# Kernel tuning notes

Measured on AMD Instinct MI355X. Metric: run time of the kernel, lower is better.

The kernel has to match this reference:

```python
import jax, jax.numpy as jnp
import numpy as np

B, T, DIN, DOUT, RANK, UDIM = 4, 2048, 4096, 4096, 2, 16

def setup_inputs() -> dict:
    key = jax.random.key(0)
    ks = jax.random.split(key, 8)
    return {
        "x": jax.random.normal(ks[0], (B, T, DIN), jnp.float32),
        "W": jax.random.normal(ks[1], (DOUT, DIN), jnp.float32) * 0.02,
        "b": jax.random.normal(ks[2], (DOUT,), jnp.float32) * 0.02,
        "U": jax.random.normal(ks[3], (DOUT, RANK), jnp.float32) * 0.02,
        "S": jax.random.normal(ks[4], (RANK, RANK), jnp.float32),
        "Vh": jax.random.normal(ks[5], (RANK, DIN), jnp.float32) * 0.02,
        "P": jax.random.normal(ks[6], (UDIM, RANK, RANK), jnp.float32),
        "v": jax.random.normal(ks[7], (UDIM,), jnp.float32),
    }

def reference(x, W, b, U, S, Vh, P, v):
    # R = sum_u v[u] * P[u]  (intended meaning of einsum('u,urr->rr'))
    R = jnp.einsum('u,uab->ab', v, P)                 # [rank, rank]
    base = jnp.einsum('btd,od->bto', x, W) + b        # frozen linear
    # x @ delta_W.T with delta_W = U @ S @ R @ Vh, chained low-rank:
    M = U @ S @ R                                     # [out, rank]
    t = jnp.einsum('btd,rd->btr', x, Vh)              # [B, T, rank]
    delta = jnp.einsum('btr,or->bto', t, M)           # [B, T, out]
    return base + delta
```

## Files before the change

kernel.cpp:

```cpp
#include <hip/hip_runtime.h>
#include <hip/hip_bf16.h>
#include <stdint.h>

typedef __hip_bfloat16 bf16;
typedef __attribute__((ext_vector_type(8))) short bf16x8;
typedef __attribute__((ext_vector_type(4))) float f32x4;

static constexpr int Mtot = 8192;
static constexpr int Ktot = 4096;
static constexpr int Ntot = 4096;
static constexpr int BM = 128, BN = 128, BK = 32;
static constexpr int NK = Ktot / BK;
static constexpr int CAST_BLOCKS = (Mtot * Ktot / 8) / 256;
static constexpr int PREP_BLOCKS = (Ntot * Ktot / 8) / 256;

__device__ __forceinline__ void gl_lds16(const void* g, void* l) {
  __builtin_amdgcn_global_load_lds(
      (const __attribute__((address_space(1))) void*)g,
      (__attribute__((address_space(3))) void*)l,
      16, 0, 0);
}

__device__ __forceinline__ uint32_t bf16pair(float a, float b) {
  __hip_bfloat16 ha = __float2bfloat16(a), hb = __float2bfloat16(b);
  uint16_t ia, ib;
  __builtin_memcpy(&ia, &ha, 2);
  __builtin_memcpy(&ib, &hb, 2);
  return (uint32_t)ia | ((uint32_t)ib << 16);
}

__global__ __launch_bounds__(256) void prep_kernel(const float* __restrict__ x,
                                                   bf16* __restrict__ xb,
                                                   const float* __restrict__ W,
                                                   const float* __restrict__ U,
                                                   const float* __restrict__ S,
                                                   const float* __restrict__ Vh,
                                                   const float* __restrict__ P,
                                                   const float* __restrict__ v,
                                                   bf16* __restrict__ Wp) {
  const int bid = blockIdx.x;
  if (bid < CAST_BLOCKS) {
    size_t gid = (size_t)bid * 256 + threadIdx.x;
    size_t d0 = gid * 8;
    const float4 a = ((const float4*)(x + d0))[0];
    const float4 b = ((const float4*)(x + d0))[1];
    uint4 pk;
    pk.x = bf16pair(a.x, a.y);
    pk.y = bf16pair(a.z, a.w);
    pk.z = bf16pair(b.x, b.y);
    pk.w = bf16pair(b.z, b.w);
    ((uint4*)(xb + d0))[0] = pk;
  } else {
    float R0 = 0.f, R1 = 0.f, R2 = 0.f, R3 = 0.f;
#pragma unroll
    for (int u = 0; u < 16; ++u) {
      float vu = v[u];
      R0 += vu * P[u * 4 + 0];
      R1 += vu * P[u * 4 + 1];
      R2 += vu * P[u * 4 + 2];
      R3 += vu * P[u * 4 + 3];
    }
    float SR00 = S[0] * R0 + S[1] * R2, SR01 = S[0] * R1 + S[1] * R3;
    float SR10 = S[2] * R0 + S[3] * R2, SR11 = S[2] * R1 + S[3] * R3;

    int gid = (bid - CAST_BLOCKS) * 256 + threadIdx.x;
    int o = gid >> 9;
    int d0 = (gid & 511) << 3;
    float u0 = U[o * 2 + 0], u1 = U[o * 2 + 1];
    float M0 = u0 * SR00 + u1 * SR10;
    float M1 = u0 * SR01 + u1 * SR11;

    const float* wrow = W + (size_t)o * Ktot + d0;
    const float4 w0 = ((const float4*)wrow)[0];
    const float4 w1 = ((const float4*)wrow)[1];
    const float4 a0 = ((const float4*)(Vh + d0))[0];
    const float4 a1 = ((const float4*)(Vh + d0))[1];
    const float4 b0 = ((const float4*)(Vh + Ktot + d0))[0];
    const float4 b1 = ((const float4*)(Vh + Ktot + d0))[1];
    float val[8];
    val[0] = w0.x + M0 * a0.x + M1 * b0.x;
    val[1] = w0.y + M0 * a0.y + M1 * b0.y;
    val[2] = w0.z + M0 * a0.z + M1 * b0.z;
    val[3] = w0.w + M0 * a0.w + M1 * b0.w;
    val[4] = w1.x + M0 * a1.x + M1 * b1.x;
    val[5] = w1.y + M0 * a1.y + M1 * b1.y;
    val[6] = w1.z + M0 * a1.z + M1 * b1.z;
    val[7] = w1.w + M0 * a1.w + M1 * b1.w;
    uint4 pk;
    pk.x = bf16pair(val[0], val[1]);
    pk.y = bf16pair(val[2], val[3]);
    pk.z = bf16pair(val[4], val[5]);
    pk.w = bf16pair(val[6], val[7]);
    ((uint4*)(Wp + (size_t)o * Ktot + d0))[0] = pk;
  }
}

__global__ __launch_bounds__(256) void gemm_kernel(const bf16* __restrict__ A,
                                                   const bf16* __restrict__ Bt,
                                                   const float* __restrict__ bias,
                                                   float* __restrict__ out) {
  __shared__ __align__(16) bf16 As[2][BM * BK];
  __shared__ __align__(16) bf16 Bs[2][BN * BK];

  const int tid = threadIdx.x;
  const int lane = tid & 63;
  const int wv = tid >> 6;
  const int m0 = blockIdx.y * BM;
  const int n0 = blockIdx.x * BN;

  const int lrow = lane >> 2;
  const int lk = (((lane & 3) ^ ((lrow >> 1) & 3)) << 3);

  const bf16* ga0 = A + (size_t)(m0 + wv * 32 + lrow) * Ktot + lk;
  const bf16* ga1 = ga0 + (size_t)16 * Ktot;
  const bf16* gb0 = Bt + (size_t)(n0 + wv * 32 + lrow) * Ktot + lk;
  const bf16* gb1 = gb0 + (size_t)16 * Ktot;
  const int laoff0 = (wv * 32) * BK;
  const int laoff1 = (wv * 32 + 16) * BK;

  const int moff = (wv >> 1) * 64;
  const int noff = (wv & 1) * 64;
  const int fm = lane & 15;
  const int q = lane >> 4;
  const int sw = ((q ^ ((fm >> 1) & 3)) << 3);

  f32x4 acc[4][4];
#pragma unroll
  for (int i = 0; i < 4; ++i)
#pragma unroll
    for (int j = 0; j < 4; ++j) acc[i][j] = {0.f, 0.f, 0.f, 0.f};

  gl_lds16(ga0, &As[0][laoff0]);
  gl_lds16(ga1, &As[0][laoff1]);
  gl_lds16(gb0, &Bs[0][laoff0]);
  gl_lds16(gb1, &Bs[0][laoff1]);
  ga0 += BK; ga1 += BK; gb0 += BK; gb1 += BK;
  __syncthreads();

  for (int kt = 0; kt < NK; ++kt) {
    const int cur = kt & 1;
    if (kt + 1 < NK) {
      const int nxt = cur ^ 1;
      gl_lds16(ga0, &As[nxt][laoff0]);
      gl_lds16(ga1, &As[nxt][laoff1]);
      gl_lds16(gb0, &Bs[nxt][laoff0]);
      gl_lds16(gb1, &Bs[nxt][laoff1]);
      ga0 += BK; ga1 += BK; gb0 += BK; gb1 += BK;
    }

    const bf16* pa = &As[cur][0];
    const bf16* pb = &Bs[cur][0];
    bf16x8 av[4], bv[4];
#pragma unroll
    for (int i = 0; i < 4; ++i)
      av[i] = *(const bf16x8*)(pa + (moff + i * 16 + fm) * BK + sw);
#pragma unroll
    for (int j = 0; j < 4; ++j)
      bv[j] = *(const bf16x8*)(pb + (noff + j * 16 + fm) * BK + sw);
#pragma unroll
    for (int i = 0; i < 4; ++i)
#pragma unroll
      for (int j = 0; j < 4; ++j)
        acc[i][j] = __builtin_amdgcn_mfma_f32_16x16x32_bf16(av[i], bv[j], acc[i][j], 0, 0, 0);

    __syncthreads();
  }

#pragma unroll
  for (int j = 0; j < 4; ++j) {
    const int gn = n0 + noff + j * 16 + fm;
    const float bj = bias[gn];
#pragma unroll
    for (int i = 0; i < 4; ++i) {
      const int gm = m0 + moff + i * 16 + q * 4;
#pragma unroll
      for (int r = 0; r < 4; ++r) {
        out[(size_t)(gm + r) * Ntot + gn] = acc[i][j][r] + bj;
      }
    }
  }
}

extern "C" void kernel_launch(void* const* d_in, const int* in_sizes, int n_in,
                              void* d_out, int out_size, void* d_ws, size_t ws_size,
                              hipStream_t stream) {
  const float* x  = (const float*)d_in[0];
  const float* W  = (const float*)d_in[1];
  const float* b  = (const float*)d_in[2];
  const float* U  = (const float*)d_in[3];
  const float* S  = (const float*)d_in[4];
  const float* Vh = (const float*)d_in[5];
  const float* P  = (const float*)d_in[6];
  const float* v  = (const float*)d_in[7];
  float* out = (float*)d_out;

  bf16* xb = (bf16*)d_ws;
  bf16* Wp = (bf16*)((char*)d_ws + (size_t)Mtot * Ktot * 2);

  prep_kernel<<<CAST_BLOCKS + PREP_BLOCKS, 256, 0, stream>>>(x, xb, W, U, S, Vh, P, v, Wp);

  dim3 grid(Ntot / BN, Mtot / BM);
  gemm_kernel<<<grid, 256, 0, stream>>>(xb, Wp, b, out);
}
```

Measured before the change: 621.6 us.

## Rewrite GEMM with 256x256x64 tiles, 8 waves, and finely interleaved ping-pong pipeline

The bf16 GEMM is restructured to use 256x256 tiles with BK=64 and 512 threads (8 waves, 2x4 layout, 128x64 per wave). Loads are staged as quarter-tiles interleaved with MFMA quadrants, synchronised by explicit barriers, waitcnts, sched_barriers and setprio. Blocks are remapped through an XCD-aware swizzle and a new XOR LDS swizzle is applied. This aims to raise arithmetic intensity and overlap global-to-LDS traffic with MFMA work, at the cost of higher register pressure, many barriers, and fragile hand-scheduled wait counts.

```diff
diff --git a/kernel.cpp b/kernel.cpp
--- a/kernel.cpp
+++ b/kernel.cpp
@@ -9,8 +9,8 @@
 static constexpr int Mtot = 8192;
 static constexpr int Ktot = 4096;
 static constexpr int Ntot = 4096;
-static constexpr int BM = 128, BN = 128, BK = 32;
-static constexpr int NK = Ktot / BK;
+static constexpr int BM = 256, BN = 256, BK = 64;
+static constexpr int NKT = Ktot / BK;
 static constexpr int CAST_BLOCKS = (Mtot * Ktot / 8) / 256;
 static constexpr int PREP_BLOCKS = (Ntot * Ktot / 8) / 256;
 
@@ -95,90 +95,154 @@
   }
 }
 
-__global__ __launch_bounds__(256) void gemm_kernel(const bf16* __restrict__ A,
-                                                   const bf16* __restrict__ Bt,
-                                                   const float* __restrict__ bias,
-                                                   float* __restrict__ out) {
+
+#define SCHEDB __builtin_amdgcn_sched_barrier(0)
+#define BAR do { SCHEDB; __builtin_amdgcn_s_barrier(); SCHEDB; } while (0)
+#define LG0 do { asm volatile("s_waitcnt lgkmcnt(0)" ::: "memory"); SCHEDB; } while (0)
+#define LG8 do { asm volatile("s_waitcnt lgkmcnt(8)" ::: "memory"); } while (0)
+#define WVM(n) do { asm volatile("s_waitcnt vmcnt(" #n ")" ::: "memory"); } while (0)
+
+__global__ __launch_bounds__(512, 2) void gemm_kernel(const bf16* __restrict__ A,
+                                                      const bf16* __restrict__ Bt,
+                                                      const float* __restrict__ bias,
+                                                      float* __restrict__ out) {
   __shared__ __align__(16) bf16 As[2][BM * BK];
   __shared__ __align__(16) bf16 Bs[2][BN * BK];
 
-  const int tid = threadIdx.x;
+  const int tid = (int)threadIdx.x;
   const int lane = tid & 63;
-  const int wv = tid >> 6;
-  const int m0 = blockIdx.y * BM;
-  const int n0 = blockIdx.x * BN;
-
-  const int lrow = lane >> 2;
-  const int lk = (((lane & 3) ^ ((lrow >> 1) & 3)) << 3);
-
-  const bf16* ga0 = A + (size_t)(m0 + wv * 32 + lrow) * Ktot + lk;
-  const bf16* ga1 = ga0 + (size_t)16 * Ktot;
-  const bf16* gb0 = Bt + (size_t)(n0 + wv * 32 + lrow) * Ktot + lk;
-  const bf16* gb1 = gb0 + (size_t)16 * Ktot;
-  const int laoff0 = (wv * 32) * BK;
-  const int laoff1 = (wv * 32 + 16) * BK;
-
-  const int moff = (wv >> 1) * 64;
-  const int noff = (wv & 1) * 64;
+  const int w = tid >> 6;
+  const int wr = w >> 2;
+  const int wc = w & 3;
+
+  int bid = (int)blockIdx.x;
+  bid = (bid & 7) * 64 + (bid >> 3);
+  const int m0 = (bid >> 4) * BM;
+  const int n0 = (bid & 15) * BN;
+
+  const int l8 = lane >> 3;
+  const int swcol = ((lane & 7) ^ l8) << 3;
+  const bf16* gA = A + (size_t)(m0 + w * 16 + l8) * Ktot + swcol;
+  const bf16* gB = Bt + (size_t)(n0 + w * 16 + l8) * Ktot + swcol;
+
   const int fm = lane & 15;
   const int q = lane >> 4;
-  const int sw = ((q ^ ((fm >> 1) & 3)) << 3);
-
-  f32x4 acc[4][4];
-#pragma unroll
-  for (int i = 0; i < 4; ++i)
+  const int rx = (fm & 7) << 4;
+  const int clo = (q * 16) ^ (rx & 48);
+  const int aoff0 = (wr * 128 + fm) * 128 + clo + (rx & 64);
+  const int aoff1 = (wr * 128 + fm) * 128 + clo + (64 ^ (rx & 64));
+  const int boff0 = (wc * 64 + fm) * 128 + clo + (rx & 64);
+  const int boff1 = (wc * 64 + fm) * 128 + clo + (64 ^ (rx & 64));
+
+#define STA(BUF, half, kt) do { \
+    const bf16* _g = gA + (size_t)((half) * 128) * Ktot + (kt) * 64; \
+    char* _l = (char*)(&As[BUF][0]) + (half) * 16384 + w * 2048; \
+    gl_lds16(_g, _l); \
+    gl_lds16(_g + (size_t)8 * Ktot, _l + 1024); \
+  } while (0)
+#define STB(BUF, half, kt) do { \
+    const bf16* _g = gB + (size_t)((half) * 128) * Ktot + (kt) * 64; \
+    char* _l = (char*)(&Bs[BUF][0]) + (half) * 16384 + w * 2048; \
+    gl_lds16(_g, _l); \
+    gl_lds16(_g + (size_t)8 * Ktot, _l + 1024); \
+  } while (0)
+#define STAGE_H(BUF, h, kt) do { \
+    if ((h) == 0) STA(BUF, 0, kt); else if ((h) == 1) STA(BUF, 1, kt); \
+    else if ((h) == 2) STB(BUF, 0, kt); else STB(BUF, 1, kt); } while (0)
+
+#define RD_A(dst, BUF, mh) do { \
+    const char* _p = (const char*)(&As[BUF][0]) + (mh) * 8192; \
+    _Pragma("unroll") for (int _i = 0; _i < 4; ++_i) { \
+      dst[_i][0] = *(const bf16x8*)(_p + _i * 2048 + aoff0); \
+      dst[_i][1] = *(const bf16x8*)(_p + _i * 2048 + aoff1); \
+    } } while (0)
+#define RD_B(dst, BUF, nh) do { \
+    const char* _p = (const char*)(&Bs[BUF][0]) + (nh) * 4096; \
+    _Pragma("unroll") for (int _j = 0; _j < 2; ++_j) { \
+      dst[_j][0] = *(const bf16x8*)(_p + _j * 2048 + boff0); \
+      dst[_j][1] = *(const bf16x8*)(_p + _j * 2048 + boff1); \
+    } } while (0)
+
+#define MFMA_Q(AV, BV, MH, NH) do { \
+    __builtin_amdgcn_s_setprio(1); \
+    _Pragma("unroll") for (int _i = 0; _i < 4; ++_i) \
+    _Pragma("unroll") for (int _j = 0; _j < 2; ++_j) { \
+      acc[(MH) * 4 + _i][(NH) * 2 + _j] = __builtin_amdgcn_mfma_f32_16x16x32_bf16( \
+          AV[_i][0], BV[_j][0], acc[(MH) * 4 + _i][(NH) * 2 + _j], 0, 0, 0); \
+      acc[(MH) * 4 + _i][(NH) * 2 + _j] = __builtin_amdgcn_mfma_f32_16x16x32_bf16( \
+          AV[_i][1], BV[_j][1], acc[(MH) * 4 + _i][(NH) * 2 + _j], 0, 0, 0); \
+    } \
+    __builtin_amdgcn_s_setprio(0); \
+  } while (0)
+
+  f32x4 acc[8][4];
+#pragma unroll
+  for (int i = 0; i < 8; ++i)
 #pragma unroll
     for (int j = 0; j < 4; ++j) acc[i][j] = {0.f, 0.f, 0.f, 0.f};
 
-  gl_lds16(ga0, &As[0][laoff0]);
-  gl_lds16(ga1, &As[0][laoff1]);
-  gl_lds16(gb0, &Bs[0][laoff0]);
-  gl_lds16(gb1, &Bs[0][laoff1]);
-  ga0 += BK; ga1 += BK; gb0 += BK; gb1 += BK;
-  __syncthreads();
-
-  for (int kt = 0; kt < NK; ++kt) {
-    const int cur = kt & 1;
-    if (kt + 1 < NK) {
-      const int nxt = cur ^ 1;
-      gl_lds16(ga0, &As[nxt][laoff0]);
-      gl_lds16(ga1, &As[nxt][laoff1]);
-      gl_lds16(gb0, &Bs[nxt][laoff0]);
-      gl_lds16(gb1, &Bs[nxt][laoff1]);
-      ga0 += BK; ga1 += BK; gb0 += BK; gb1 += BK;
-    }
-
-    const bf16* pa = &As[cur][0];
-    const bf16* pb = &Bs[cur][0];
-    bf16x8 av[4], bv[4];
-#pragma unroll
-    for (int i = 0; i < 4; ++i)
-      av[i] = *(const bf16x8*)(pa + (moff + i * 16 + fm) * BK + sw);
-#pragma unroll
-    for (int j = 0; j < 4; ++j)
-      bv[j] = *(const bf16x8*)(pb + (noff + j * 16 + fm) * BK + sw);
-#pragma unroll
-    for (int i = 0; i < 4; ++i)
-#pragma unroll
-      for (int j = 0; j < 4; ++j)
-        acc[i][j] = __builtin_amdgcn_mfma_f32_16x16x32_bf16(av[i], bv[j], acc[i][j], 0, 0, 0);
-
-    __syncthreads();
+  bf16x8 a[4][2], b0[2][2], b1[2][2];
+
+  STAGE_H(0, 0, 0); STAGE_H(0, 1, 0); STAGE_H(0, 2, 0); STAGE_H(0, 3, 0);
+  STAGE_H(1, 2, 1); STAGE_H(1, 3, 1); STAGE_H(1, 0, 1);
+  WVM(6);
+  BAR;
+
+  for (int it = 0; it < 31; ++it) {
+    const int k1 = 2 * it + 1;
+    const int k2 = 2 * it + 2;
+    const int k3 = 2 * it + 3;
+    RD_A(a, 0, 0); RD_B(b0, 0, 0); STAGE_H(1, 1, k1); LG8;
+    BAR; LG0; MFMA_Q(a, b0, 0, 0); BAR;
+    RD_B(b1, 0, 1);
+    BAR; LG0; MFMA_Q(a, b1, 0, 1); BAR;
+    RD_A(a, 0, 1); STAGE_H(0, 2, k2);
+    BAR; LG0; MFMA_Q(a, b0, 1, 0); BAR;
+    STAGE_H(0, 3, k2);
+    BAR; MFMA_Q(a, b1, 1, 1); SCHEDB; WVM(4); BAR;
+    RD_A(a, 1, 0); RD_B(b0, 1, 0); STAGE_H(0, 0, k2); LG8;
+    BAR; LG0; MFMA_Q(a, b0, 0, 0); BAR;
+    RD_B(b1, 1, 1); STAGE_H(0, 1, k2);
+    BAR; LG0; MFMA_Q(a, b1, 0, 1); BAR;
+    RD_A(a, 1, 1); STAGE_H(1, 2, k3);
+    BAR; LG0; MFMA_Q(a, b0, 1, 0); BAR;
+    STAGE_H(1, 3, k3); STAGE_H(1, 0, k3);
+    BAR; MFMA_Q(a, b1, 1, 1); SCHEDB; WVM(6); BAR;
   }
 
-#pragma unroll
-  for (int j = 0; j < 4; ++j) {
-    const int gn = n0 + noff + j * 16 + fm;
+  RD_A(a, 0, 0); RD_B(b0, 0, 0); STAGE_H(1, 1, 63); LG8;
+  BAR; LG0; MFMA_Q(a, b0, 0, 0); BAR;
+  RD_B(b1, 0, 1);
+  BAR; LG0; MFMA_Q(a, b1, 0, 1); BAR;
+  RD_A(a, 0, 1);
+  BAR; LG0; MFMA_Q(a, b0, 1, 0); BAR;
+  BAR; MFMA_Q(a, b1, 1, 1); SCHEDB; WVM(0); BAR;
+  RD_A(a, 1, 0); RD_B(b0, 1, 0);
+  BAR; LG0; MFMA_Q(a, b0, 0, 0); BAR;
+  RD_B(b1, 1, 1);
+  BAR; LG0; MFMA_Q(a, b1, 0, 1); BAR;
+  RD_A(a, 1, 1);
+  BAR; LG0; MFMA_Q(a, b0, 1, 0); BAR;
+  MFMA_Q(a, b1, 1, 1);
+
+#pragma unroll
+  for (int jb = 0; jb < 4; ++jb) {
+    const int gn = n0 + wc * 64 + jb * 16 + fm;
     const float bj = bias[gn];
 #pragma unroll
-    for (int i = 0; i < 4; ++i) {
-      const int gm = m0 + moff + i * 16 + q * 4;
-#pragma unroll
-      for (int r = 0; r < 4; ++r) {
-        out[(size_t)(gm + r) * Ntot + gn] = acc[i][j][r] + bj;
-      }
+    for (int ia = 0; ia < 8; ++ia) {
+      float* o = out + (size_t)(m0 + wr * 128 + ia * 16 + q * 4) * Ntot + gn;
+#pragma unroll
+      for (int r = 0; r < 4; ++r) o[(size_t)r * Ntot] = acc[ia][jb][r] + bj;
     }
   }
+
+#undef STA
+#undef STB
+#undef STAGE_H
+#undef RD_A
+#undef RD_B
+#undef MFMA_Q
 }
 
 extern "C" void kernel_launch(void* const* d_in, const int* in_sizes, int n_in,
@@ -199,6 +263,6 @@
 
   prep_kernel<<<CAST_BLOCKS + PREP_BLOCKS, 256, 0, stream>>>(x, xb, W, U, S, Vh, P, v, Wp);
 
-  dim3 grid(Ntot / BN, Mtot / BM);
-  gemm_kernel<<<grid, 256, 0, stream>>>(xb, Wp, b, out);
-}
+  dim3 grid(Mtot / BM * (Ntot / BN));
+  gemm_kernel<<<grid, 512, 0, stream>>>(xb, Wp, b, out);
+}
```

Result: faster. 531.9 us (-14.4%).
